# Optimization experiments

Measured on AMD Instinct MI355X. Metric: run time of the kernel, lower is better.

## Reference

```python
import jax, jax.numpy as jnp
import numpy as np

B, S, D = 4, 2048, 1024
H = 16
HS = D // H  # 64


def setup_inputs() -> dict:
    key = jax.random.key(0)
    ks = jax.random.split(key, 6)
    scale = 1.0 / np.sqrt(D)
    x = jax.random.normal(ks[0], (B, S, D), dtype=jnp.float32)
    # per-head projection weights, stacked: [H, D, HS]
    Wq = jax.random.normal(ks[1], (H, D, HS), dtype=jnp.float32) * scale
    Wk = jax.random.normal(ks[2], (H, D, HS), dtype=jnp.float32) * scale
    Wv = jax.random.normal(ks[3], (H, D, HS), dtype=jnp.float32) * scale
    Wo = jax.random.normal(ks[4], (D, D), dtype=jnp.float32) * scale
    bo = jax.random.normal(ks[5], (D,), dtype=jnp.float32) * 0.01
    return {"x": x, "Wq": Wq, "Wk": Wk, "Wv": Wv, "Wo": Wo, "bo": bo}


def reference(x, Wq, Wk, Wv, Wo, bo):
    # Per-head dense projections (no bias): [B,S,D] x [H,D,HS] -> [B,H,S,HS]
    q = jnp.einsum('bsd,hde->bhse', x, Wq)
    k = jnp.einsum('bsd,hde->bhse', x, Wk)
    v = jnp.einsum('bsd,hde->bhse', x, Wv)
    # scaled dot-product scores: [B,H,S,S]
    scores = jnp.einsum('bhse,bhte->bhst', q, k) / jnp.sqrt(jnp.asarray(HS, dtype=x.dtype))
    # causal mask (lower triangular kept)
    causal = jnp.tril(jnp.ones((S, S), dtype=bool))
    scores = jnp.where(causal, scores, -jnp.inf)
    attn = jax.nn.softmax(scores, axis=-1)
    # dropout is identity at inference (rate handled as 0)
    out = jnp.einsum('bhst,bhte->bhse', attn, v)  # [B,H,S,HS]
    # concat heads: [B,S,H*HS] = [B,S,D]
    out = jnp.transpose(out, (0, 2, 1, 3)).reshape(B, S, D)
    return out @ Wo + bo
```

## Files before the change

### kernel.cpp

```cpp
#include <hip/hip_runtime.h>
#include <hip/hip_bf16.h>
#include <stdint.h>

#define NB 4
#define NS 2048
#define ND 1024
#define NH 16
#define NHS 64
#define NEG_BIG (-1e30f)
#define Q_SCALE 0.18033688011112042f

typedef __bf16 bf16x8 __attribute__((ext_vector_type(8)));
typedef float floatx4 __attribute__((ext_vector_type(4)));
typedef short s16x4 __attribute__((ext_vector_type(4)));

#if defined(__has_builtin)
#if __has_builtin(__builtin_amdgcn_mfma_f32_16x16x16bf16_1k)
#define HAVE_MFMA1K 1
#endif
#endif
#ifndef HAVE_MFMA1K
#define HAVE_MFMA1K 0
#endif

static constexpr size_t WSLAB = (size_t)NH * ND * NHS;
static constexpr size_t QSLAB = (size_t)NB * NH * NS * NHS;
static constexpr size_t XSLAB = (size_t)NB * NS * ND;

__device__ __forceinline__ uint16_t f2b(float f) {
    union { __hip_bfloat16 h; uint16_t u; } cv;
    cv.h = __float2bfloat16(f);
    return cv.u;
}

__device__ __forceinline__ void gll16(const void* g, void* l) {
  __builtin_amdgcn_global_load_lds(
      (__attribute__((address_space(1))) void*)(uintptr_t)g,
      (__attribute__((address_space(3))) void*)(uintptr_t)l,
      16, 0, 0);
}

__global__ __launch_bounds__(256) void k_prep(
    const float* __restrict__ x, const float* __restrict__ Wq,
    const float* __restrict__ Wk, const float* __restrict__ Wv,
    const float* __restrict__ Wo, uint16_t* __restrict__ xb,
    uint16_t* __restrict__ wt) {
  __shared__ __align__(16) uint16_t T[64][72];
  int bid = blockIdx.x;
  int tid = threadIdx.x;
  if (bid < 4096) {
    size_t i0 = ((size_t)bid * 256 + tid) * 8;
    float4 f0 = *(const float4*)&x[i0];
    float4 f1 = *(const float4*)&x[i0 + 4];
    __align__(16) uint16_t tmp[8];
    tmp[0] = f2b(f0.x); tmp[1] = f2b(f0.y); tmp[2] = f2b(f0.z); tmp[3] = f2b(f0.w);
    tmp[4] = f2b(f1.x); tmp[5] = f2b(f1.y); tmp[6] = f2b(f1.z); tmp[7] = f2b(f1.w);
    *(uint4*)&xb[i0] = *(uint4*)tmp;
    return;
  }
  bid -= 4096;
  const float* src; uint16_t* dst;
  int srcStride, dstStride, r0, c0;
  if (bid < 768) {
    int mat = bid >> 8;
    int rem = bid & 255;
    int h = rem >> 4, dt = rem & 15;
    const float* W = (mat == 0) ? Wq : (mat == 1) ? Wk : Wv;
    src = W + (size_t)h * (ND * NHS);
    dst = wt + (size_t)mat * WSLAB + (size_t)h * (NHS * ND);
    srcStride = NHS; dstStride = ND;
    r0 = dt * 64; c0 = 0;
  } else {
    int rem = bid - 768;
    int dt = rem >> 4, et = rem & 15;
    src = Wo; dst = wt + 3 * WSLAB;
    srcStride = ND; dstStride = ND;
    r0 = dt * 64; c0 = et * 64;
  }
  for (int u = tid; u < 1024; u += 256) {
    int row = u >> 4, cq = u & 15;
    float4 f = *(const float4*)&src[(size_t)(r0 + row) * srcStride + c0 + cq * 4];
    uint16_t* p = &T[row][cq * 4];
    p[0] = f2b(f.x); p[1] = f2b(f.y); p[2] = f2b(f.z); p[3] = f2b(f.w);
  }
  __syncthreads();
  for (int u = tid; u < 512; u += 256) {
    int c = u >> 3, cg = u & 7;
    __align__(16) uint16_t tmp[8];
    for (int j = 0; j < 8; j++) tmp[j] = T[cg * 8 + j][c];
    *(uint4*)&dst[(size_t)(c0 + c) * dstStride + r0 + cg * 8] = *(uint4*)tmp;
  }
}

__global__ __launch_bounds__(512, 4) void k_qkv(
    const uint16_t* __restrict__ xb, const uint16_t* __restrict__ wt,
    uint16_t* __restrict__ qk, uint16_t* __restrict__ vt) {
  __shared__ __align__(16) uint16_t L[32768];

  int bid = blockIdx.x;
  int xcd = bid & 7, idx = bid >> 3;
  int mtile = xcd * 8 + (idx & 7);
  int ntile = idx >> 3;
  int m0 = mtile * 128;
  int n0 = ntile * 128;

  int tid = threadIdx.x;
  int wave = tid >> 6, lane = tid & 63, quad = lane >> 4, l16 = lane & 15;
  int wr = wave >> 2, wc = wave & 3;

  int swc = ((tid & 3) ^ ((tid >> 4) & 3)) * 8;
  const uint16_t* pA = xb + (size_t)(m0 + (tid >> 2)) * ND + swc;
  const uint16_t* pB = wt + (size_t)(n0 + (tid >> 2)) * ND + swc;
  const int stOff = wave * 512;

  const int rq = (quad ^ (l16 >> 2)) * 8;
  const int offA = (wr * 64 + l16) * 32 + rq;
  const int offB = (wc * 32 + l16) * 32 + rq;

  floatx4 acc[4][2];
  #pragma unroll
  for (int i = 0; i < 4; i++)
    #pragma unroll
    for (int j = 0; j < 2; j++) acc[i][j] = (floatx4){0.f, 0.f, 0.f, 0.f};

#define STAGE(A_)                                                               \
  do {                                                                          \
    int a_ = (A_);                                                              \
    if (a_ < 32) {                                                              \
      int ko_ = (a_ >> 1) * 64 + (a_ & 1) * 32;                                 \
      gll16(pA + ko_, &L[(a_ & 3) * 4096 + stOff]);                             \
      gll16(pB + ko_, &L[16384 + (a_ & 3) * 4096 + stOff]);                     \
    }                                                                           \
  } while (0)

#define PH_BAR()                         \
  do {                                   \
    asm volatile("" ::: "memory");       \
    __builtin_amdgcn_s_barrier();        \
    asm volatile("" ::: "memory");       \
  } while (0)

  STAGE(0); STAGE(1); STAGE(2);
  asm volatile("s_waitcnt vmcnt(4)" ::: "memory");
  PH_BAR();

#define MFMA8()                                                                           \
  _Pragma("unroll")                                                                       \
  for (int mt_ = 0; mt_ < 4; mt_++)                                                       \
    _Pragma("unroll")                                                                     \
    for (int nt_ = 0; nt_ < 2; nt_++)                                                     \
      acc[mt_][nt_] = __builtin_amdgcn_mfma_f32_16x16x32_bf16(af[mt_], bfr[nt_], acc[mt_][nt_], 0, 0, 0)

  for (int t = 0; t < 16; ++t) {
    {
      int sA = ((2 * t) & 3) * 4096;
      int sB = 16384 + ((2 * t) & 3) * 4096;
      bf16x8 af[4], bfr[2];
      #pragma unroll
      for (int i = 0; i < 4; i++) af[i] = *(const bf16x8*)&L[sA + offA + i * 512];
      #pragma unroll
      for (int i = 0; i < 2; i++) bfr[i] = *(const bf16x8*)&L[sB + offB + i * 512];
      STAGE(2 * t + 3);
      PH_BAR();
      __builtin_amdgcn_s_setprio(1);
      MFMA8();
      __builtin_amdgcn_s_setprio(0);
      if (t < 15) { asm volatile("s_waitcnt vmcnt(4)" ::: "memory"); }
      else        { asm volatile("s_waitcnt vmcnt(0)" ::: "memory"); }
      PH_BAR();
    }
    {
      int sA = ((2 * t + 1) & 3) * 4096;
      int sB = 16384 + ((2 * t + 1) & 3) * 4096;
      bf16x8 af[4], bfr[2];
      #pragma unroll
      for (int i = 0; i < 4; i++) af[i] = *(const bf16x8*)&L[sA + offA + i * 512];
      #pragma unroll
      for (int i = 0; i < 2; i++) bfr[i] = *(const bf16x8*)&L[sB + offB + i * 512];
      STAGE(2 * t + 4);
      PH_BAR();
      __builtin_amdgcn_s_setprio(1);
      MFMA8();
      __builtin_amdgcn_s_setprio(0);
      if (t < 14)       { asm volatile("s_waitcnt vmcnt(4)" ::: "memory"); }
      else if (t == 14) { asm volatile("s_waitcnt vmcnt(2)" ::: "memory"); }
      if (t < 15) PH_BAR();
    }
  }
#undef MFMA8
#undef STAGE
#undef PH_BAR

  int matid = n0 >> 10;
  int b = m0 >> 11;
  if (matid == 2) {
    int hh = ((n0 - 2048) >> 6) + (wc >> 1);
    #pragma unroll
    for (int nt = 0; nt < 2; nt++) {
      int e = (wc & 1) * 32 + nt * 16 + l16;
      uint16_t* vrow = vt + ((size_t)(b * 16 + hh) * 64 + e) * NS;
      #pragma unroll
      for (int mt = 0; mt < 4; mt++) {
        __align__(8) uint16_t t4v[4];
        #pragma unroll
        for (int r = 0; r < 4; r++) t4v[r] = f2b(acc[mt][nt][r]);
        int s = (m0 & 2047) + wr * 64 + mt * 16 + quad * 4;
        *(uint2*)&vrow[s] = *(uint2*)t4v;
      }
    }
  } else {
    float scale = (matid == 0) ? Q_SCALE : 1.0f;
    uint16_t* base = qk + (size_t)matid * QSLAB;
    int hh = ((n0 & 1023) >> 6) + (wc >> 1);
    #pragma unroll
    for (int mt = 0; mt < 4; mt++) {
      int s = (m0 & 2047) + wr * 64 + mt * 16 + quad * 4;
      size_t rbase = ((size_t)(b * 16 + hh) * NS + s) * NHS;
      #pragma unroll
      for (int nt = 0; nt < 2; nt++)
        #pragma unroll
        for (int r = 0; r < 4; r++)
          base[rbase + (size_t)r * NHS + (wc & 1) * 32 + nt * 16 + l16] =
              f2b(acc[mt][nt][r] * scale);
    }
  }
}

#if HAVE_MFMA1K
__global__ __launch_bounds__(256, 4) void k_attn(
    const uint16_t* __restrict__ Q, const uint16_t* __restrict__ K,
    const uint16_t* __restrict__ VT, uint16_t* __restrict__ Y) {
  __shared__ __align__(16) uint16_t Ks[64][72];
  __shared__ __align__(16) uint16_t Vs[64][72];
  int bh = blockIdx.y;
  int b = bh >> 4, h = bh & 15;
  int ta = blockIdx.x;
  int tb = 31 - ta;
  const uint16_t* Qp = Q + (size_t)bh * (NS * NHS);
  const uint16_t* Kp = K + (size_t)bh * (NS * NHS);
  const uint16_t* Vp = VT + (size_t)bh * (NS * NHS);
  int tid = threadIdx.x;
  int wv = tid >> 6, lane = tid & 63, quad = lane >> 4, l16 = lane & 15;

  int row0 = tid >> 3, cg0 = tid & 7;
  int row1 = (tid + 256) >> 3, cg1 = tid & 7;

  int rA = ta * 64 + wv * 16 + l16;
  int rB = tb * 64 + wv * 16 + l16;
  bf16x8 aqA0 = *(const bf16x8*)&Qp[(size_t)rA * NHS + quad * 8];
  bf16x8 aqA1 = *(const bf16x8*)&Qp[(size_t)rA * NHS + 32 + quad * 8];
  bf16x8 aqB0 = *(const bf16x8*)&Qp[(size_t)rB * NHS + quad * 8];
  bf16x8 aqB1 = *(const bf16x8*)&Qp[(size_t)rB * NHS + 32 + quad * 8];

  float lAs = 0.f, lBs = 0.f;
  floatx4 oA[4], oB[4];
  for (int et = 0; et < 4; et++) {
    oA[et] = (floatx4){0.f, 0.f, 0.f, 0.f};
    oB[et] = (floatx4){0.f, 0.f, 0.f, 0.f};
  }

  uint4 rk0, rk1, rv0, rv1;
  rk0 = *(const uint4*)&Kp[(size_t)(0 * 64 + row0) * NHS + cg0 * 8];
  rk1 = *(const uint4*)&Kp[(size_t)(0 * 64 + row1) * NHS + cg1 * 8];
  rv0 = *(const uint4*)&Vp[(size_t)row0 * NS + 0 * 64 + cg0 * 8];
  rv1 = *(const uint4*)&Vp[(size_t)row1 * NS + 0 * 64 + cg1 * 8];

  for (int kt = 0; kt <= tb; kt++) {
    bool doA = (kt <= ta);
    __syncthreads();
    *(uint4*)&Ks[row0][cg0 * 8] = rk0;
    *(uint4*)&Ks[row1][cg1 * 8] = rk1;
    *(uint4*)&Vs[row0][cg0 * 8] = rv0;
    *(uint4*)&Vs[row1][cg1 * 8] = rv1;
    __syncthreads();
    if (kt < tb) {
      rk0 = *(const uint4*)&Kp[(size_t)((kt + 1) * 64 + row0) * NHS + cg0 * 8];
      rk1 = *(const uint4*)&Kp[(size_t)((kt + 1) * 64 + row1) * NHS + cg1 * 8];
      rv0 = *(const uint4*)&Vp[(size_t)row0 * NS + (kt + 1) * 64 + cg0 * 8];
      rv1 = *(const uint4*)&Vp[(size_t)row1 * NS + (kt + 1) * 64 + cg1 * 8];
    }

    s16x4 pbA[4], pbB[4];
    for (int ct = 0; ct < 4; ct++) {
      bf16x8 kb0 = *(const bf16x8*)&Ks[ct * 16 + l16][quad * 8];
      bf16x8 kb1 = *(const bf16x8*)&Ks[ct * 16 + l16][32 + quad * 8];
      int key = kt * 64 + ct * 16 + quad * 4;
      floatx4 c = (floatx4){0.f, 0.f, 0.f, 0.f};
      c = __builtin_amdgcn_mfma_f32_16x16x32_bf16(kb0, aqB0, c, 0, 0, 0);
      c = __builtin_amdgcn_mfma_f32_16x16x32_bf16(kb1, aqB1, c, 0, 0, 0);
      for (int r = 0; r < 4; r++) {
        float s = (kt == tb && key + r > rB) ? NEG_BIG : c[r];
        float p = __builtin_amdgcn_exp2f(s);
        lBs += p;
        pbB[ct][r] = (short)f2b(p);
      }
      if (doA) {
        floatx4 d = (floatx4){0.f, 0.f, 0.f, 0.f};
        d = __builtin_amdgcn_mfma_f32_16x16x32_bf16(kb0, aqA0, d, 0, 0, 0);
        d = __builtin_amdgcn_mfma_f32_16x16x32_bf16(kb1, aqA1, d, 0, 0, 0);
        for (int r = 0; r < 4; r++) {
          float s = (kt == ta && key + r > rA) ? NEG_BIG : d[r];
          float p = __builtin_amdgcn_exp2f(s);
          lAs += p;
          pbA[ct][r] = (short)f2b(p);
        }
      }
    }
    for (int et = 0; et < 4; et++)
      for (int ct = 0; ct < 4; ct++) {
        s16x4 va = *(const s16x4*)&Vs[et * 16 + l16][ct * 16 + quad * 4];
        oB[et] = __builtin_amdgcn_mfma_f32_16x16x16bf16_1k(va, pbB[ct], oB[et], 0, 0, 0);
        if (doA)
          oA[et] = __builtin_amdgcn_mfma_f32_16x16x16bf16_1k(va, pbA[ct], oA[et], 0, 0, 0);
      }
  }
  lAs += __shfl_xor(lAs, 16, 64); lAs += __shfl_xor(lAs, 32, 64);
  lBs += __shfl_xor(lBs, 16, 64); lBs += __shfl_xor(lBs, 32, 64);
  float invA = 1.f / lAs, invB = 1.f / lBs;
  uint16_t* yb = Y + (size_t)b * NS * ND + (size_t)h * NHS;
  for (int et = 0; et < 4; et++) {
    __align__(8) uint16_t tA[4], tB[4];
    for (int r = 0; r < 4; r++) {
      tA[r] = f2b(oA[et][r] * invA);
      tB[r] = f2b(oB[et][r] * invB);
    }
    *(uint2*)&yb[(size_t)rA * ND + et * 16 + quad * 4] = *(uint2*)tA;
    *(uint2*)&yb[(size_t)rB * ND + et * 16 + quad * 4] = *(uint2*)tB;
  }
}
#else
__global__ __launch_bounds__(256) void k_attn(
    const uint16_t* __restrict__ Q, const uint16_t* __restrict__ K,
    const uint16_t* __restrict__ VT, uint16_t* __restrict__ Y) {
  __shared__ __align__(16) uint16_t Ks[64][72];
  __shared__ __align__(16) uint16_t Vs[64][72];
  __shared__ __align__(16) uint16_t Ps[4][2][16][72];
  int bh = blockIdx.y;
  int b = bh >> 4, h = bh & 15;
  int ta = blockIdx.x;
  int tb = 31 - ta;
  const uint16_t* Qp = Q + (size_t)bh * (NS * NHS);
  const uint16_t* Kp = K + (size_t)bh * (NS * NHS);
  const uint16_t* Vp = VT + (size_t)bh * (NS * NHS);
  int tid = threadIdx.x;
  int wv = tid >> 6, lane = tid & 63, quad = lane >> 4, l16 = lane & 15;

  int rA = ta * 64 + wv * 16 + l16;
  int rB = tb * 64 + wv * 16 + l16;
  bf16x8 aqA0 = *(const bf16x8*)&Qp[(size_t)rA * NHS + quad * 8];
  bf16x8 aqA1 = *(const bf16x8*)&Qp[(size_t)rA * NHS + 32 + quad * 8];
  bf16x8 aqB0 = *(const bf16x8*)&Qp[(size_t)rB * NHS + quad * 8];
  bf16x8 aqB1 = *(const bf16x8*)&Qp[(size_t)rB * NHS + 32 + quad * 8];

  float lA[4] = {0.f, 0.f, 0.f, 0.f}, lB[4] = {0.f, 0.f, 0.f, 0.f};
  floatx4 oA[4], oB[4];
  for (int ct = 0; ct < 4; ct++) {
    oA[ct] = (floatx4){0.f, 0.f, 0.f, 0.f};
    oB[ct] = (floatx4){0.f, 0.f, 0.f, 0.f};
  }
  for (int kt = 0; kt <= tb; kt++) {
    bool doA = (kt <= ta);
    __syncthreads();
    for (int u = tid; u < 512; u += 256) {
      int row = u >> 3, cg = u & 7;
      *(uint4*)&Ks[row][cg * 8] =
          *(const uint4*)&Kp[(size_t)(kt * 64 + row) * NHS + cg * 8];
    }
    for (int u = tid; u < 512; u += 256) {
      int row = u >> 3, cg = u & 7;
      *(uint4*)&Vs[row][cg * 8] =
          *(const uint4*)&Vp[(size_t)row * NS + kt * 64 + cg * 8];
    }
    __syncthreads();
    floatx4 sA[4], sB[4];
    for (int ct = 0; ct < 4; ct++) {
      bf16x8 kb0 = *(const bf16x8*)&Ks[ct * 16 + l16][quad * 8];
      bf16x8 kb1 = *(const bf16x8*)&Ks[ct * 16 + l16][32 + quad * 8];
      floatx4 c = (floatx4){0.f, 0.f, 0.f, 0.f};
      c = __builtin_amdgcn_mfma_f32_16x16x32_bf16(aqB0, kb0, c, 0, 0, 0);
      c = __builtin_amdgcn_mfma_f32_16x16x32_bf16(aqB1, kb1, c, 0, 0, 0);
      sB[ct] = c;
      if (doA) {
        floatx4 d = (floatx4){0.f, 0.f, 0.f, 0.f};
        d = __builtin_amdgcn_mfma_f32_16x16x32_bf16(aqA0, kb0, d, 0, 0, 0);
        d = __builtin_amdgcn_mfma_f32_16x16x32_bf16(aqA1, kb1, d, 0, 0, 0);
        sA[ct] = d;
      }
    }
    if (kt == tb) {
      int qrb = tb * 64 + wv * 16 + quad * 4;
      for (int ct = 0; ct < 4; ct++) {
        int kg = kt * 64 + ct * 16 + l16;
        for (int r = 0; r < 4; r++)
          sB[ct][r] = (kg <= qrb + r) ? sB[ct][r] : NEG_BIG;
      }
    }
    if (doA && kt == ta) {
      int qrb = ta * 64 + wv * 16 + quad * 4;
      for (int ct = 0; ct < 4; ct++) {
        int kg = kt * 64 + ct * 16 + l16;
        for (int r = 0; r < 4; r++)
          sA[ct][r] = (kg <= qrb + r) ? sA[ct][r] : NEG_BIG;
      }
    }
    for (int ct = 0; ct < 4; ct++)
      for (int r = 0; r < 4; r++) {
        float p = __builtin_amdgcn_exp2f(sB[ct][r]);
        lB[r] += p;
        Ps[wv][1][quad * 4 + r][ct * 16 + l16] = f2b(p);
      }
    if (doA)
      for (int ct = 0; ct < 4; ct++)
        for (int r = 0; r < 4; r++) {
          float p = __builtin_amdgcn_exp2f(sA[ct][r]);
          lA[r] += p;
          Ps[wv][0][quad * 4 + r][ct * 16 + l16] = f2b(p);
        }
    bf16x8 apB0 = *(const bf16x8*)&Ps[wv][1][l16][quad * 8];
    bf16x8 apB1 = *(const bf16x8*)&Ps[wv][1][l16][32 + quad * 8];
    bf16x8 apA0, apA1;
    if (doA) {
      apA0 = *(const bf16x8*)&Ps[wv][0][l16][quad * 8];
      apA1 = *(const bf16x8*)&Ps[wv][0][l16][32 + quad * 8];
    }
    for (int ct = 0; ct < 4; ct++) {
      bf16x8 vb0 = *(const bf16x8*)&Vs[ct * 16 + l16][quad * 8];
      bf16x8 vb1 = *(const bf16x8*)&Vs[ct * 16 + l16][32 + quad * 8];
      oB[ct] = __builtin_amdgcn_mfma_f32_16x16x32_bf16(apB0, vb0, oB[ct], 0, 0, 0);
      oB[ct] = __builtin_amdgcn_mfma_f32_16x16x32_bf16(apB1, vb1, oB[ct], 0, 0, 0);
      if (doA) {
        oA[ct] = __builtin_amdgcn_mfma_f32_16x16x32_bf16(apA0, vb0, oA[ct], 0, 0, 0);
        oA[ct] = __builtin_amdgcn_mfma_f32_16x16x32_bf16(apA1, vb1, oA[ct], 0, 0, 0);
      }
    }
  }
  for (int off = 1; off < 16; off <<= 1)
    for (int r = 0; r < 4; r++) {
      lA[r] += __shfl_xor(lA[r], off, 64);
      lB[r] += __shfl_xor(lB[r], off, 64);
    }
  uint16_t* yb = Y + (size_t)b * NS * ND + (size_t)h * NHS;
  for (int ct = 0; ct < 4; ct++)
    for (int r = 0; r < 4; r++) {
      int sA_ = ta * 64 + wv * 16 + quad * 4 + r;
      int sB_ = tb * 64 + wv * 16 + quad * 4 + r;
      yb[(size_t)sA_ * ND + ct * 16 + l16] = f2b(oA[ct][r] / lA[r]);
      yb[(size_t)sB_ * ND + ct * 16 + l16] = f2b(oB[ct][r] / lB[r]);
    }
}
#endif

__global__ __launch_bounds__(512, 4) void k_proj(
    const uint16_t* __restrict__ y, const uint16_t* __restrict__ wot,
    const float* __restrict__ bo, float* __restrict__ out) {
  __shared__ __align__(16) uint16_t L[32768];

  int bid = blockIdx.x;
  int xcd = bid & 7, idx = bid >> 3;
  int mtile = xcd * 8 + (idx & 7);
  int ntile = idx >> 3;
  int m0 = mtile * 128;
  int n0 = ntile * 128;

  int tid = threadIdx.x;
  int wave = tid >> 6, lane = tid & 63, quad = lane >> 4, l16 = lane & 15;
  int wr = wave >> 2, wc = wave & 3;

  int swc = ((tid & 3) ^ ((tid >> 4) & 3)) * 8;
  const uint16_t* pA = y + (size_t)(m0 + (tid >> 2)) * ND + swc;
  const uint16_t* pB = wot + (size_t)(n0 + (tid >> 2)) * ND + swc;
  const int stOff = wave * 512;

  const int rq = (quad ^ (l16 >> 2)) * 8;
  const int offA = (wr * 64 + l16) * 32 + rq;
  const int offB = (wc * 32 + l16) * 32 + rq;

  floatx4 acc[4][2];
  #pragma unroll
  for (int i = 0; i < 4; i++)
    #pragma unroll
    for (int j = 0; j < 2; j++) acc[i][j] = (floatx4){0.f, 0.f, 0.f, 0.f};

#define STAGE(A_)                                                               \
  do {                                                                          \
    int a_ = (A_);                                                              \
    if (a_ < 32) {                                                              \
      int ko_ = (a_ >> 1) * 64 + (a_ & 1) * 32;                                 \
      gll16(pA + ko_, &L[(a_ & 3) * 4096 + stOff]);                             \
      gll16(pB + ko_, &L[16384 + (a_ & 3) * 4096 + stOff]);                     \
    }                                                                           \
  } while (0)

#define PH_BAR()                         \
  do {                                   \
    asm volatile("" ::: "memory");       \
    __builtin_amdgcn_s_barrier();        \
    asm volatile("" ::: "memory");       \
  } while (0)

  STAGE(0); STAGE(1); STAGE(2);
  asm volatile("s_waitcnt vmcnt(4)" ::: "memory");
  PH_BAR();

#define MFMA8()                                                                           \
  _Pragma("unroll")                                                                       \
  for (int mt_ = 0; mt_ < 4; mt_++)                                                       \
    _Pragma("unroll")                                                                     \
    for (int nt_ = 0; nt_ < 2; nt_++)                                                     \
      acc[mt_][nt_] = __builtin_amdgcn_mfma_f32_16x16x32_bf16(af[mt_], bfr[nt_], acc[mt_][nt_], 0, 0, 0)

  for (int t = 0; t < 16; ++t) {
    {
      int sA = ((2 * t) & 3) * 4096;
      int sB = 16384 + ((2 * t) & 3) * 4096;
      bf16x8 af[4], bfr[2];
      #pragma unroll
      for (int i = 0; i < 4; i++) af[i] = *(const bf16x8*)&L[sA + offA + i * 512];
      #pragma unroll
      for (int i = 0; i < 2; i++) bfr[i] = *(const bf16x8*)&L[sB + offB + i * 512];
      STAGE(2 * t + 3);
      PH_BAR();
      __builtin_amdgcn_s_setprio(1);
      MFMA8();
      __builtin_amdgcn_s_setprio(0);
      if (t < 15) { asm volatile("s_waitcnt vmcnt(4)" ::: "memory"); }
      else        { asm volatile("s_waitcnt vmcnt(0)" ::: "memory"); }
      PH_BAR();
    }
    {
      int sA = ((2 * t + 1) & 3) * 4096;
      int sB = 16384 + ((2 * t + 1) & 3) * 4096;
      bf16x8 af[4], bfr[2];
      #pragma unroll
      for (int i = 0; i < 4; i++) af[i] = *(const bf16x8*)&L[sA + offA + i * 512];
      #pragma unroll
      for (int i = 0; i < 2; i++) bfr[i] = *(const bf16x8*)&L[sB + offB + i * 512];
      STAGE(2 * t + 4);
      PH_BAR();
      __builtin_amdgcn_s_setprio(1);
      MFMA8();
      __builtin_amdgcn_s_setprio(0);
      if (t < 14)       { asm volatile("s_waitcnt vmcnt(4)" ::: "memory"); }
      else if (t == 14) { asm volatile("s_waitcnt vmcnt(2)" ::: "memory"); }
      if (t < 15) PH_BAR();
    }
  }
#undef MFMA8
#undef STAGE
#undef PH_BAR

  float bv[2];
  #pragma unroll
  for (int nt = 0; nt < 2; nt++) bv[nt] = bo[n0 + wc * 32 + nt * 16 + l16];
  #pragma unroll
  for (int mt = 0; mt < 4; mt++) {
    int s = m0 + wr * 64 + mt * 16 + quad * 4;
    #pragma unroll
    for (int nt = 0; nt < 2; nt++) {
      int n = n0 + wc * 32 + nt * 16 + l16;
      #pragma unroll
      for (int r = 0; r < 4; r++)
        out[(size_t)(s + r) * ND + n] = acc[mt][nt][r] + bv[nt];
    }
  }
}

extern "C" void kernel_launch(void* const* d_in, const int* in_sizes, int n_in,
                              void* d_out, int out_size, void* d_ws, size_t ws_size,
                              hipStream_t stream) {
  const float* x  = (const float*)d_in[0];
  const float* Wq = (const float*)d_in[1];
  const float* Wk = (const float*)d_in[2];
  const float* Wv = (const float*)d_in[3];
  const float* Wo = (const float*)d_in[4];
  const float* bo = (const float*)d_in[5];
  uint16_t* ws = (uint16_t*)d_ws;

  uint16_t* wt = ws;
  uint16_t* xb = ws + 4 * WSLAB;
  uint16_t* q  = xb + XSLAB;
  uint16_t* k  = q + QSLAB;
  uint16_t* vt = k + QSLAB;
  uint16_t* y  = vt + QSLAB;

  k_prep<<<dim3(5120), dim3(256), 0, stream>>>(x, Wq, Wk, Wv, Wo, xb, wt);
  k_qkv<<<dim3(1536), dim3(512), 0, stream>>>(xb, wt, q, vt);
  k_attn<<<dim3(16, NB * NH), dim3(256), 0, stream>>>(q, k, vt, y);
  k_proj<<<dim3(512), dim3(512), 0, stream>>>(y, wt + 3 * WSLAB, bo, (float*)d_out);
}
```

Measured before the change: 253.7 us.

## Double-buffer K/V tiles in LDS with direct global-to-LDS loads and XOR swizzle

The attention kernel now stages K and V tiles straight from global memory into two LDS buffers using a gll16 helper (presumably a global_load_lds path), prefetching tile kt+1 while tile kt is computed. This replaces register staging and its two barriers per iteration with a single barrier. The padded 72-wide layout becomes an unpadded 64-wide layout with an XOR swizzle to avoid bank conflicts, and the inner loops get explicit unroll pragmas. LDS use doubles and correctness depends on the async loads having landed before the barrier (wait counts).

```diff
diff --git a/kernel.cpp b/kernel.cpp
--- a/kernel.cpp
+++ b/kernel.cpp
@@ -230,8 +230,8 @@
 __global__ __launch_bounds__(256, 4) void k_attn(
     const uint16_t* __restrict__ Q, const uint16_t* __restrict__ K,
     const uint16_t* __restrict__ VT, uint16_t* __restrict__ Y) {
-  __shared__ __align__(16) uint16_t Ks[64][72];
-  __shared__ __align__(16) uint16_t Vs[64][72];
+  __shared__ __align__(16) uint16_t Ks[2][4096];
+  __shared__ __align__(16) uint16_t Vs[2][4096];
   int bh = blockIdx.y;
   int b = bh >> 4, h = bh & 15;
   int ta = blockIdx.x;
@@ -242,8 +242,31 @@
   int tid = threadIdx.x;
   int wv = tid >> 6, lane = tid & 63, quad = lane >> 4, l16 = lane & 15;
 
-  int row0 = tid >> 3, cg0 = tid & 7;
-  int row1 = (tid + 256) >> 3, cg1 = tid & 7;
+  int srow = lane >> 3;
+  int swOff = ((lane & 7) ^ srow) * 8;
+  int stRow0 = wv * 16 + srow;
+  int stRow1 = wv * 16 + 8 + srow;
+  const int dst0 = wv * 1024;
+  const int dst1 = wv * 1024 + 512;
+
+#define STAGE_KV(KT, BUF)                                                         \
+  do {                                                                            \
+    int kt_ = (KT);                                                               \
+    gll16(Kp + (size_t)(kt_ * 64 + stRow0) * NHS + swOff, &Ks[BUF][dst0]);        \
+    gll16(Kp + (size_t)(kt_ * 64 + stRow1) * NHS + swOff, &Ks[BUF][dst1]);        \
+    gll16(Vp + (size_t)stRow0 * NS + kt_ * 64 + swOff, &Vs[BUF][dst0]);           \
+    gll16(Vp + (size_t)stRow1 * NS + kt_ * 64 + swOff, &Vs[BUF][dst1]);           \
+  } while (0)
+
+  int e3 = l16 & 7;
+  int kc0 = (quad ^ e3) * 8;
+  int kc1 = ((4 | quad) ^ e3) * 8;
+  int vql = (quad & 1) * 4;
+  int vqh = quad >> 1;
+  int vcol[4];
+  #pragma unroll
+  for (int ct = 0; ct < 4; ct++)
+    vcol[ct] = (((ct * 2 + vqh) ^ e3) * 8) + vql;
 
   int rA = ta * 64 + wv * 16 + l16;
   int rB = tb * 64 + wv * 16 + l16;
@@ -259,35 +282,27 @@
     oB[et] = (floatx4){0.f, 0.f, 0.f, 0.f};
   }
 
-  uint4 rk0, rk1, rv0, rv1;
-  rk0 = *(const uint4*)&Kp[(size_t)(0 * 64 + row0) * NHS + cg0 * 8];
-  rk1 = *(const uint4*)&Kp[(size_t)(0 * 64 + row1) * NHS + cg1 * 8];
-  rv0 = *(const uint4*)&Vp[(size_t)row0 * NS + 0 * 64 + cg0 * 8];
-  rv1 = *(const uint4*)&Vp[(size_t)row1 * NS + 0 * 64 + cg1 * 8];
+  STAGE_KV(0, 0);
+  __syncthreads();
 
   for (int kt = 0; kt <= tb; kt++) {
+    int cur = kt & 1;
+    if (kt < tb) STAGE_KV(kt + 1, cur ^ 1);
+    const uint16_t* KB = &Ks[cur][0];
+    const uint16_t* VB = &Vs[cur][0];
     bool doA = (kt <= ta);
-    __syncthreads();
-    *(uint4*)&Ks[row0][cg0 * 8] = rk0;
-    *(uint4*)&Ks[row1][cg1 * 8] = rk1;
-    *(uint4*)&Vs[row0][cg0 * 8] = rv0;
-    *(uint4*)&Vs[row1][cg1 * 8] = rv1;
-    __syncthreads();
-    if (kt < tb) {
-      rk0 = *(const uint4*)&Kp[(size_t)((kt + 1) * 64 + row0) * NHS + cg0 * 8];
-      rk1 = *(const uint4*)&Kp[(size_t)((kt + 1) * 64 + row1) * NHS + cg1 * 8];
-      rv0 = *(const uint4*)&Vp[(size_t)row0 * NS + (kt + 1) * 64 + cg0 * 8];
-      rv1 = *(const uint4*)&Vp[(size_t)row1 * NS + (kt + 1) * 64 + cg1 * 8];
-    }
 
     s16x4 pbA[4], pbB[4];
+    #pragma unroll
     for (int ct = 0; ct < 4; ct++) {
-      bf16x8 kb0 = *(const bf16x8*)&Ks[ct * 16 + l16][quad * 8];
-      bf16x8 kb1 = *(const bf16x8*)&Ks[ct * 16 + l16][32 + quad * 8];
+      int krow = (ct * 16 + l16) * 64;
+      bf16x8 kb0 = *(const bf16x8*)&KB[krow + kc0];
+      bf16x8 kb1 = *(const bf16x8*)&KB[krow + kc1];
       int key = kt * 64 + ct * 16 + quad * 4;
       floatx4 c = (floatx4){0.f, 0.f, 0.f, 0.f};
       c = __builtin_amdgcn_mfma_f32_16x16x32_bf16(kb0, aqB0, c, 0, 0, 0);
       c = __builtin_amdgcn_mfma_f32_16x16x32_bf16(kb1, aqB1, c, 0, 0, 0);
+      #pragma unroll
       for (int r = 0; r < 4; r++) {
         float s = (kt == tb && key + r > rB) ? NEG_BIG : c[r];
         float p = __builtin_amdgcn_exp2f(s);
@@ -298,6 +313,7 @@
         floatx4 d = (floatx4){0.f, 0.f, 0.f, 0.f};
         d = __builtin_amdgcn_mfma_f32_16x16x32_bf16(kb0, aqA0, d, 0, 0, 0);
         d = __builtin_amdgcn_mfma_f32_16x16x32_bf16(kb1, aqA1, d, 0, 0, 0);
+        #pragma unroll
         for (int r = 0; r < 4; r++) {
           float s = (kt == ta && key + r > rA) ? NEG_BIG : d[r];
           float p = __builtin_amdgcn_exp2f(s);
@@ -306,14 +322,21 @@
         }
       }
     }
-    for (int et = 0; et < 4; et++)
+    #pragma unroll
+    for (int et = 0; et < 4; et++) {
+      int vrow = (et * 16 + l16) * 64;
+      #pragma unroll
       for (int ct = 0; ct < 4; ct++) {
-        s16x4 va = *(const s16x4*)&Vs[et * 16 + l16][ct * 16 + quad * 4];
+        s16x4 va = *(const s16x4*)&VB[vrow + vcol[ct]];
         oB[et] = __builtin_amdgcn_mfma_f32_16x16x16bf16_1k(va, pbB[ct], oB[et], 0, 0, 0);
         if (doA)
           oA[et] = __builtin_amdgcn_mfma_f32_16x16x16bf16_1k(va, pbA[ct], oA[et], 0, 0, 0);
       }
-  }
+    }
+    __syncthreads();
+  }
+#undef STAGE_KV
+
   lAs += __shfl_xor(lAs, 16, 64); lAs += __shfl_xor(lAs, 32, 64);
   lBs += __shfl_xor(lBs, 16, 64); lBs += __shfl_xor(lBs, 32, 64);
   float invA = 1.f / lAs, invB = 1.f / lBs;
```

New measurement: 250.6 us (median of 2 runs). Within noise of the previous version (-1.2%).
